# Performance work log

Measured on AMD Instinct MI355X. Metric: run time of the kernel, lower is better.

The kernel has to match this reference:

```python
import jax, jax.numpy as jnp
import numpy as np

B, S, D, H, R = 2, 2048, 1024, 16, 4
HD = D // H  # 64


def _linear_params(key, din, dout):
    k1, k2 = jax.random.split(key)
    bound = 1.0 / np.sqrt(din)
    w = jax.random.uniform(k1, (din, dout), jnp.float32, -bound, bound)
    b = jax.random.uniform(k2, (dout,), jnp.float32, -bound, bound)
    return w, b


def setup_inputs() -> dict:
    key = jax.random.key(0)
    ks = jax.random.split(key, 10)
    x = jax.random.normal(ks[0], (B, S, D), jnp.float32)
    wq_p, bq_p = _linear_params(ks[1], D, D)
    wk_p, bk_p = _linear_params(ks[2], D, D)
    wv_p, bv_p = _linear_params(ks[3], D, D)
    wo_p, bo_p = _linear_params(ks[4], D, D)
    wq_s, bq_s = _linear_params(ks[5], D, H * R)
    wk_s, bk_s = _linear_params(ks[6], D, H * R)
    wv_s, bv_s = _linear_params(ks[7], D, H * R)
    wo_s, bo_s = _linear_params(ks[8], H * R, D)
    w_cross = jnp.float32(-0.1)
    return {"x": x,
            "wq_p": wq_p, "bq_p": bq_p, "wk_p": wk_p, "bk_p": bk_p,
            "wv_p": wv_p, "bv_p": bv_p, "wo_p": wo_p, "bo_p": bo_p,
            "wq_s": wq_s, "bq_s": bq_s, "wk_s": wk_s, "bk_s": bk_s,
            "wv_s": wv_s, "bv_s": bv_s, "wo_s": wo_s, "bo_s": bo_s,
            "w_cross": w_cross}


def _mha(x, wq, bq, wk, bk, wv, bv, dh, scale):
    b, s, _ = x.shape
    q = (x @ wq + bq).reshape(b, s, H, dh)
    k = (x @ wk + bk).reshape(b, s, H, dh)
    v = (x @ wv + bv).reshape(b, s, H, dh)
    scores = jnp.einsum('bqhd,bkhd->bhqk', q, k) / scale
    attn = jax.nn.softmax(scores, axis=-1)
    out = jnp.einsum('bhqk,bkhd->bqhd', attn, v)
    return out.reshape(b, s, H * dh)


def reference(x, wq_p, bq_p, wk_p, bk_p, wv_p, bv_p, wo_p, bo_p,
              wq_s, bq_s, wk_s, bk_s, wv_s, bv_s, wo_s, bo_s, w_cross):
    primary = _mha(x, wq_p, bq_p, wk_p, bk_p, wv_p, bv_p, HD, np.sqrt(HD)) @ wo_p + bo_p
    secondary = _mha(x, wq_s, bq_s, wk_s, bk_s, wv_s, bv_s, R, np.sqrt(R)) @ wo_s + bo_s
    return primary + w_cross * secondary
```

## Files before the change

### kernel.cpp

```cpp
#include <hip/hip_runtime.h>
#include <stdint.h>

typedef unsigned short u16;
typedef __bf16 bf16x8 __attribute__((ext_vector_type(8)));
typedef float f32x4 __attribute__((ext_vector_type(4)));
typedef u16 u16x8 __attribute__((ext_vector_type(8)));
typedef u16 u16x4 __attribute__((ext_vector_type(4)));
typedef unsigned u32x4 __attribute__((ext_vector_type(4)));


__device__ __forceinline__ u16 f2bf(float f) {
  unsigned u = __builtin_bit_cast(unsigned, f);
  u += 0x7FFFu + ((u >> 16) & 1u);
  return (u16)(u >> 16);
}
__device__ __forceinline__ unsigned cvtpk(float lo, float hi) {
  unsigned r;
  asm("v_cvt_pk_bf16_f32 %0, %1, %2" : "=v"(r) : "v"(lo), "v"(hi));
  return r;
}
__device__ __forceinline__ void gld_lds16(const void* g, void* l) {
  __builtin_amdgcn_global_load_lds((__attribute__((address_space(1))) void*)(g),
                                   (__attribute__((address_space(3))) void*)(l),
                                   16, 0, 0);
}

__global__ __launch_bounds__(256)
void k_prep(const float* __restrict__ x,
            const float* __restrict__ wq_p, const float* __restrict__ wk_p,
            const float* __restrict__ wv_p, const float* __restrict__ wo_p,
            const float* __restrict__ wq_s, const float* __restrict__ wk_s,
            const float* __restrict__ wv_s, const float* __restrict__ wo_s,
            const float* __restrict__ bq_p, const float* __restrict__ bk_p,
            const float* __restrict__ bq_s, const float* __restrict__ bk_s,
            const float* __restrict__ bo_p, const float* __restrict__ bo_s,
            const float* __restrict__ wcr,
            u16* __restrict__ xb, u16* __restrict__ Wall, u16* __restrict__ Wvt,
            u16* __restrict__ Wvst, u16* __restrict__ Bto,
            float* __restrict__ ballqk, float* __restrict__ bfin) {
  const int id = blockIdx.x;
  if (id < 2048) {
    const int i = id * 256 + threadIdx.x;
    const float4* p = reinterpret_cast<const float4*>(x) + (size_t)i * 2;
    float4 a = p[0], b = p[1];
    u16x8 o;
    o[0] = f2bf(a.x); o[1] = f2bf(a.y); o[2] = f2bf(a.z); o[3] = f2bf(a.w);
    o[4] = f2bf(b.x); o[5] = f2bf(b.y); o[6] = f2bf(b.z); o[7] = f2bf(b.w);
    *reinterpret_cast<u16x8*>(xb + (size_t)i * 8) = o;
    return;
  }
  if (id < 6400) {
    __shared__ float tile[32][33];
    const int tx = threadIdx.x & 31, ty = threadIdx.x >> 5;
    const float* src; u16* dst; int N, ldd, n0, k0; float sc = 1.f;
    if (id < 6144) {
      const int tid = id - 2048, job = tid >> 10, t10 = tid & 1023;
      switch (job) {
        case 0: src = wq_p; dst = Wall;                       ldd = 1024; break;
        case 1: src = wk_p; dst = Wall + (size_t)1024 * 1024; ldd = 1024; break;
        case 2: src = wv_p; dst = Wvt;                        ldd = 1024; break;
        default: src = wo_p; dst = Bto;                       ldd = 1088; break;
      }
      N = 1024; n0 = (t10 & 31) * 32; k0 = (t10 >> 5) * 32;
    } else {
      const int tid = id - 6144, job = tid >> 6, t6 = tid & 63;
      int ntx;
      switch (job) {
        case 0: src = wq_s; dst = Wall + (size_t)2048 * 1024; N = 64;   ldd = 1024; ntx = 2; break;
        case 1: src = wk_s; dst = Wall + (size_t)2112 * 1024; N = 64;   ldd = 1024; ntx = 2; break;
        case 2: src = wv_s; dst = Wvst;                       N = 64;   ldd = 1024; ntx = 2; break;
        default: src = wo_s; dst = Bto + 1024;                N = 1024; ldd = 1088; ntx = 32; sc = wcr[0]; break;
      }
      n0 = (t6 % ntx) * 32; k0 = (t6 / ntx) * 32;
    }
    #pragma unroll
    for (int i = 0; i < 4; ++i)
      tile[ty + i * 8][tx] = src[(size_t)(k0 + ty + i * 8) * N + n0 + tx];
    __syncthreads();
    #pragma unroll
    for (int i = 0; i < 4; ++i)
      dst[(size_t)(n0 + ty + i * 8) * ldd + k0 + tx] = f2bf(tile[tx][ty + i * 8] * sc);
    return;
  }
  const int i = (id - 6400) * 256 + threadIdx.x;
  if (i < 1024)       ballqk[i] = bq_p[i];
  else if (i < 2048)  ballqk[i] = bk_p[i - 1024];
  else if (i < 2112)  ballqk[i] = bq_s[i - 2048];
  else if (i < 2176)  ballqk[i] = bk_s[i - 2112];
  if (i < 1024) bfin[i] = bo_p[i] + wcr[0] * bo_s[i];
}

template <int BN, int WAVES_M, int OUTMODE, int OHD>
__device__ __forceinline__
void gemm_body(const u16* __restrict__ A, int lda,
               const u16* __restrict__ Bt, int ldb,
               const float* __restrict__ bias,
               void* __restrict__ Cv, int ldc, int K,
               int bx, int by, u16* sm) {
  constexpr int WM = 128 / WAVES_M;
  constexpr int MF = WM / 16;
  u16* Atile = sm;
  u16* Btile = sm + 8192;
  const int t = threadIdx.x, w = t >> 6;
  const int lane = t & 63, l4 = lane & 15, g = lane >> 4;
  const int wr = (WAVES_M == 4) ? w : (w >> 1);
  const int wc = (WAVES_M == 4) ? 0 : (w & 1);
  const int m0 = bx * 128, n0 = by * BN;

  auto stage = [&](int buf, int kt) {
    const int k0 = kt * 32;
    #pragma unroll
    for (int r = 0; r < 2; ++r) {
      const int slot = r * 256 + t;
      const int row = slot >> 2, blk = slot & 3;
      const int srcb = blk ^ ((row >> 1) & 3);
      gld_lds16(A + (size_t)(m0 + row) * lda + k0 + srcb * 8,
                &Atile[buf * 4096 + (r * 256 + w * 64) * 8]);
    }
    #pragma unroll
    for (int r = 0; r < BN / 64; ++r) {
      const int slot = r * 256 + t;
      const int row = slot >> 2, blk = slot & 3;
      const int srcb = blk ^ ((row >> 1) & 3);
      gld_lds16(Bt + (size_t)(n0 + row) * ldb + k0 + srcb * 8,
                &Btile[buf * (BN * 32) + (r * 256 + w * 64) * 8]);
    }
  };

  const f32x4 vz = {0.f, 0.f, 0.f, 0.f};
  f32x4 acc[MF][4];
  #pragma unroll
  for (int mi = 0; mi < MF; ++mi)
    #pragma unroll
    for (int ni = 0; ni < 4; ++ni) acc[mi][ni] = vz;

  const int nkt = K >> 5;
  stage(0, 0);
  __syncthreads();
  for (int kt = 0; kt < nkt; ++kt) {
    const int cur = kt & 1;
    if (kt + 1 < nkt) stage(cur ^ 1, kt + 1);
    bf16x8 af[MF], bfv[4];
    #pragma unroll
    for (int mi = 0; mi < MF; ++mi) {
      const int row = wr * WM + mi * 16 + l4;
      const int blk = g ^ ((row >> 1) & 3);
      af[mi] = *reinterpret_cast<const bf16x8*>(&Atile[cur * 4096 + row * 32 + blk * 8]);
    }
    #pragma unroll
    for (int ni = 0; ni < 4; ++ni) {
      const int row = wc * 64 + ni * 16 + l4;
      const int blk = g ^ ((row >> 1) & 3);
      bfv[ni] = *reinterpret_cast<const bf16x8*>(&Btile[cur * (BN * 32) + row * 32 + blk * 8]);
    }
    #pragma unroll
    for (int mi = 0; mi < MF; ++mi)
      #pragma unroll
      for (int ni = 0; ni < 4; ++ni)
        acc[mi][ni] = __builtin_amdgcn_mfma_f32_16x16x32_bf16(af[mi], bfv[ni],
                                                              acc[mi][ni], 0, 0, 0);
    __syncthreads();
  }
  #pragma unroll
  for (int mi = 0; mi < MF; ++mi) {
    #pragma unroll
    for (int ni = 0; ni < 4; ++ni) {
      const int grow0 = m0 + wr * WM + mi * 16 + g * 4;
      const int gcol = n0 + wc * 64 + ni * 16 + l4;
      const float bb = bias ? bias[gcol] : 0.f;
      if constexpr (OUTMODE == 1) {
        const int bidx = grow0 >> 11, s0 = grow0 & 2047;
        const int hh = gcol / OHD, dd = gcol % OHD;
        u16x4 ov;
        #pragma unroll
        for (int r = 0; r < 4; ++r) ov[r] = f2bf(acc[mi][ni][r] + bb);
        *reinterpret_cast<u16x4*>((u16*)Cv +
            (size_t)((bidx * 16 + hh) * OHD + dd) * 2048 + s0) = ov;
      } else {
        #pragma unroll
        for (int r = 0; r < 4; ++r) {
          const float v = acc[mi][ni][r] + bb;
          if constexpr (OUTMODE == 0)
            ((u16*)Cv)[(size_t)(grow0 + r) * ldc + gcol] = f2bf(v);
          else
            ((float*)Cv)[(size_t)(grow0 + r) * ldc + gcol] = v;
        }
      }
    }
  }
}

__global__ __launch_bounds__(256, 2)
void k_proj3(const u16* __restrict__ xb, const u16* __restrict__ Wall,
             const u16* __restrict__ Wvt, const u16* __restrict__ Wvst,
             const float* __restrict__ ballqk, const float* __restrict__ bv_p,
             const float* __restrict__ bv_s,
             u16* __restrict__ QKs, u16* __restrict__ Vpt, u16* __restrict__ Vst) {
  __shared__ __attribute__((aligned(16))) u16 sm[16384];
  const int id = blockIdx.x;
  if (id < 544) {
    gemm_body<128, 2, 0, 64>(xb, 1024, Wall, 1024, ballqk, QKs, 2176, 1024,
                             id & 31, id >> 5, sm);
  } else if (id < 800) {
    const int lid = id - 544;
    gemm_body<128, 2, 1, 64>(xb, 1024, Wvt, 1024, bv_p, Vpt, 0, 1024,
                             lid & 31, lid >> 5, sm);
  } else {
    const int lid = id - 800;
    gemm_body<64, 4, 1, 4>(xb, 1024, Wvst, 1024, bv_s, Vst, 0, 1024,
                           lid & 31, lid >> 5, sm);
  }
}

__global__ __launch_bounds__(256, 2)
void k_gemm_final(const u16* __restrict__ A, const u16* __restrict__ Bt,
                  const float* __restrict__ bias, float* __restrict__ C) {
  __shared__ __attribute__((aligned(16))) u16 sm[16384];
  gemm_body<128, 2, 2, 64>(A, 1088, Bt, 1088, bias, C, 1024, 1088,
                           blockIdx.x, blockIdx.y, sm);
}

__global__ __launch_bounds__(256, 2)
void k_attn(const u16* __restrict__ QKs, const u16* __restrict__ Vpt,
            const u16* __restrict__ Vst, u16* __restrict__ Ao) {
  __shared__ __attribute__((aligned(16))) u16 sm[26664];
  const int t = threadIdx.x, w = t >> 6;
  const int lane = t & 63, l4 = lane & 15, g = lane >> 4;
  const int grp = blockIdx.x >> 3, sub = blockIdx.x & 7;

  if ((grp & 1) == 0) {
    u16* Klds = sm;
    u16* Vlds = sm + 8192;
    const int id = (grp >> 1) * 8 + sub;
    const int lin = (id & 7) * 64 + (id >> 3);
    const int qt = lin & 15, hb = lin >> 4;
    const int h = hb & 15, b = hb >> 4;
    const int q0 = qt * 128;

    const u16* Qbase = QKs + (size_t)(b * 2048 + q0) * 2176 + h * 64;
    const u16* Kbase = QKs + (size_t)(b * 2048) * 2176 + 1024 + h * 64;
    const u16* Vbase = Vpt + (size_t)((b * 16 + h) * 64) * 2048;

    #pragma unroll
    for (int r = 0; r < 2; ++r) {
      const int sl = r * 256 + t, row = sl >> 3, blk = sl & 7;
      const int srcb = blk ^ (row & 7);
      const int prow = (row & 32) | (((row >> 2) & 3) << 3) | (((row >> 4) & 1) << 2) | (row & 3);
      gld_lds16(Kbase + (size_t)prow * 2176 + srcb * 8, &Klds[(r * 256 + w * 64) * 8]);
      gld_lds16(Vbase + (size_t)row * 2048 + srcb * 8, &Vlds[(r * 256 + w * 64) * 8]);
    }

    bf16x8 aq[2][2];
    #pragma unroll
    for (int mi = 0; mi < 2; ++mi)
      #pragma unroll
      for (int kd = 0; kd < 2; ++kd)
        aq[mi][kd] = *reinterpret_cast<const bf16x8*>(
            Qbase + (size_t)(w * 32 + mi * 16 + l4) * 2176 + kd * 32 + g * 8);

    __syncthreads();

    const f32x4 vz = {0.f, 0.f, 0.f, 0.f};
    float l_r[2] = {0.f, 0.f};
    f32x4 acc_o[2][4];
    #pragma unroll
    for (int mi = 0; mi < 2; ++mi)
      #pragma unroll
      for (int nd = 0; nd < 4; ++nd) acc_o[mi][nd] = vz;

    for (int kt = 0; kt < 32; ++kt) {
      const int cur = kt & 1;
      if (kt < 31) {
        const int kn = kt + 1;
        #pragma unroll
        for (int r = 0; r < 2; ++r) {
          const int sl = r * 256 + t, row = sl >> 3, blk = sl & 7;
          const int srcb = blk ^ (row & 7);
          const int prow = (row & 32) | (((row >> 2) & 3) << 3) | (((row >> 4) & 1) << 2) | (row & 3);
          gld_lds16(Kbase + (size_t)(kn * 64 + prow) * 2176 + srcb * 8,
                    &Klds[(cur ^ 1) * 4096 + (r * 256 + w * 64) * 8]);
          gld_lds16(Vbase + (size_t)row * 2048 + kn * 64 + srcb * 8,
                    &Vlds[(cur ^ 1) * 4096 + (r * 256 + w * 64) * 8]);
        }
      }
      f32x4 sc[2][4];
      #pragma unroll
      for (int mi = 0; mi < 2; ++mi)
        #pragma unroll
        for (int ni = 0; ni < 4; ++ni) sc[mi][ni] = vz;
      #pragma unroll
      for (int kd = 0; kd < 2; ++kd) {
        bf16x8 bk[4];
        #pragma unroll
        for (int ni = 0; ni < 4; ++ni) {
          const int row = ni * 16 + l4;
          const int blk = (kd * 4 + g) ^ (row & 7);
          bk[ni] = *reinterpret_cast<const bf16x8*>(&Klds[cur * 4096 + row * 64 + blk * 8]);
        }
        __builtin_amdgcn_s_setprio(1);
        #pragma unroll
        for (int mi = 0; mi < 2; ++mi)
          #pragma unroll
          for (int ni = 0; ni < 4; ++ni)
            sc[mi][ni] = __builtin_amdgcn_mfma_f32_16x16x32_bf16(bk[ni], aq[mi][kd],
                                                                 sc[mi][ni], 0, 0, 0);
        __builtin_amdgcn_s_setprio(0);
      }
      unsigned pw[2][4][2];
      #pragma unroll
      for (int mi = 0; mi < 2; ++mi) {
        float rs = 0.f;
        #pragma unroll
        for (int ni = 0; ni < 4; ++ni) {
          const float a0 = __expf(sc[mi][ni][0] * 0.125f);
          const float a1 = __expf(sc[mi][ni][1] * 0.125f);
          const float a2 = __expf(sc[mi][ni][2] * 0.125f);
          const float a3 = __expf(sc[mi][ni][3] * 0.125f);
          rs += (a0 + a1) + (a2 + a3);
          pw[mi][ni][0] = cvtpk(a0, a1);
          pw[mi][ni][1] = cvtpk(a2, a3);
        }
        rs += __shfl_xor(rs, 16);
        rs += __shfl_xor(rs, 32);
        l_r[mi] += rs;
      }
      #pragma unroll
      for (int ks = 0; ks < 2; ++ks) {
        bf16x8 bv[4];
        #pragma unroll
        for (int nd = 0; nd < 4; ++nd) {
          const int row = nd * 16 + l4;
          const int blk = (ks * 4 + g) ^ (row & 7);
          bv[nd] = *reinterpret_cast<const bf16x8*>(&Vlds[cur * 4096 + row * 64 + blk * 8]);
        }
        __builtin_amdgcn_s_setprio(1);
        #pragma unroll
        for (int mi = 0; mi < 2; ++mi) {
          const u32x4 aw = {pw[mi][2 * ks][0], pw[mi][2 * ks][1],
                            pw[mi][2 * ks + 1][0], pw[mi][2 * ks + 1][1]};
          const bf16x8 ap = __builtin_bit_cast(bf16x8, aw);
          #pragma unroll
          for (int nd = 0; nd < 4; ++nd)
            acc_o[mi][nd] = __builtin_amdgcn_mfma_f32_16x16x32_bf16(ap, bv[nd],
                                                                    acc_o[mi][nd], 0, 0, 0);
        }
        __builtin_amdgcn_s_setprio(0);
      }
      __syncthreads();
    }
    float linv[2][4];
    #pragma unroll
    for (int mi = 0; mi < 2; ++mi)
      #pragma unroll
      for (int r = 0; r < 4; ++r) {
        const int src = (lane & 48) + ((lane & 48) >> 2) + r;
        linv[mi][r] = 1.0f / __shfl(l_r[mi], src);
      }
    #pragma unroll
    for (int mi = 0; mi < 2; ++mi)
      #pragma unroll
      for (int nd = 0; nd < 4; ++nd)
        #pragma unroll
        for (int r = 0; r < 4; ++r) {
          const int grow = b * 2048 + q0 + w * 32 + mi * 16 + g * 4 + r;
          const int gcol = h * 64 + nd * 16 + l4;
          Ao[(size_t)grow * 1088 + gcol] = f2bf(acc_o[mi][nd][r] * linv[mi][r]);
        }
    return;
  }

  u16* KsL = sm;
  u16* VtL = sm + 8192;
  u16* Plds = sm + 18472;
  const int sid = (grp >> 1) * 8 + sub;
  const int q0 = (sid & 15) * 128, h = (sid >> 4) & 15, b = sid >> 8;

  const u16* Vsrc = Vst + (size_t)((b * 16 + h) * 4) * 2048;
  #pragma unroll
  for (int r = 0; r < 4; ++r)
    gld_lds16(Vsrc + (size_t)r * 2048 + t * 8, &VtL[r * 2056 + w * 512]);
  {
    u16x8 ones;
    #pragma unroll
    for (int j = 0; j < 8; ++j) ones[j] = 0x3F80;
    *reinterpret_cast<u16x8*>(&VtL[4 * 2056 + t * 8]) = ones;
  }
  #pragma unroll
  for (int i = 0; i < 8; ++i) {
    const int s = i * 256 + t;
    const uint2 kk = *reinterpret_cast<const uint2*>(
        QKs + (size_t)(b * 2048 + s) * 2176 + 2112 + h * 4);
    *reinterpret_cast<uint2*>(&KsL[s * 4]) = kk;
  }
  bf16x8 aq[2];
  #pragma unroll
  for (int mi = 0; mi < 2; ++mi) {
    u16x8 qv = {0, 0, 0, 0, 0, 0, 0, 0};
    if (g == 0) {
      const uint2 qq = *reinterpret_cast<const uint2*>(
          QKs + (size_t)(b * 2048 + q0 + w * 32 + mi * 16 + l4) * 2176 + 2048 + h * 4);
      qv[0] = (u16)(qq.x & 0xffff); qv[1] = (u16)(qq.x >> 16);
      qv[2] = (u16)(qq.y & 0xffff); qv[3] = (u16)(qq.y >> 16);
    }
    aq[mi] = __builtin_bit_cast(bf16x8, qv);
  }
  __syncthreads();

  const f32x4 vz = {0.f, 0.f, 0.f, 0.f};
  f32x4 acc[2];
  acc[0] = vz; acc[1] = vz;

  for (int kt = 0; kt < 32; ++kt) {
    f32x4 sc[2][4];
    bf16x8 bk[4];
    #pragma unroll
    for (int ni = 0; ni < 4; ++ni) {
      u16x8 kv = {0, 0, 0, 0, 0, 0, 0, 0};
      if (g == 0) {
        const uint2 kk = *reinterpret_cast<const uint2*>(
            &KsL[(kt * 64 + ni * 16 + l4) * 4]);
        kv[0] = (u16)(kk.x & 0xffff); kv[1] = (u16)(kk.x >> 16);
        kv[2] = (u16)(kk.y & 0xffff); kv[3] = (u16)(kk.y >> 16);
      }
      bk[ni] = __builtin_bit_cast(bf16x8, kv);
    }
    #pragma unroll
    for (int mi = 0; mi < 2; ++mi)
      #pragma unroll
      for (int ni = 0; ni < 4; ++ni)
        sc[mi][ni] = __builtin_amdgcn_mfma_f32_16x16x32_bf16(aq[mi], bk[ni], vz, 0, 0, 0);
    #pragma unroll
    for (int mi = 0; mi < 2; ++mi)
      #pragma unroll
      for (int r = 0; r < 4; ++r) {
        const int prow = mi * 16 + g * 4 + r;
        #pragma unroll
        for (int ni = 0; ni < 4; ++ni) {
          const float p = __expf(sc[mi][ni][r] * 0.5f);
          const int col = ni * 16 + l4;
          Plds[w * 2048 + prow * 64 + ((col >> 3) ^ (prow & 7)) * 8 + (col & 7)] = f2bf(p);
        }
      }
    asm volatile("s_waitcnt lgkmcnt(0)" ::: "memory");
    #pragma unroll
    for (int ks = 0; ks < 2; ++ks) {
      const int blko = kt * 8 + ks * 4 + g;
      const int vrow = (l4 < 4) ? l4 : 4;
      const bf16x8 bv = *reinterpret_cast<const bf16x8*>(&VtL[vrow * 2056 + blko * 8]);
      #pragma unroll
      for (int mi = 0; mi < 2; ++mi) {
        const int row = mi * 16 + l4;
        const int blk = (ks * 4 + g) ^ (row & 7);
        const bf16x8 ap = *reinterpret_cast<const bf16x8*>(&Plds[w * 2048 + row * 64 + blk * 8]);
        acc[mi] = __builtin_amdgcn_mfma_f32_16x16x32_bf16(ap, bv, acc[mi], 0, 0, 0);
      }
    }
  }
  #pragma unroll
  for (int mi = 0; mi < 2; ++mi)
    #pragma unroll
    for (int r = 0; r < 4; ++r) {
      const float lsum = __shfl(acc[mi][r], (lane & 48) + 4);
      if (l4 < 4) {
        const int grow = b * 2048 + q0 + w * 32 + mi * 16 + g * 4 + r;
        Ao[(size_t)grow * 1088 + 1024 + h * 4 + l4] = f2bf(acc[mi][r] / lsum);
      }
    }
}

extern "C" void kernel_launch(void* const* d_in, const int* in_sizes, int n_in,
                              void* d_out, int out_size, void* d_ws, size_t ws_size,
                              hipStream_t stream) {
  (void)in_sizes; (void)n_in; (void)out_size; (void)ws_size;
  const float* x    = (const float*)d_in[0];
  const float* wq_p = (const float*)d_in[1];
  const float* bq_p = (const float*)d_in[2];
  const float* wk_p = (const float*)d_in[3];
  const float* bk_p = (const float*)d_in[4];
  const float* wv_p = (const float*)d_in[5];
  const float* bv_p = (const float*)d_in[6];
  const float* wo_p = (const float*)d_in[7];
  const float* bo_p = (const float*)d_in[8];
  const float* wq_s = (const float*)d_in[9];
  const float* bq_s = (const float*)d_in[10];
  const float* wk_s = (const float*)d_in[11];
  const float* bk_s = (const float*)d_in[12];
  const float* wv_s = (const float*)d_in[13];
  const float* bv_s = (const float*)d_in[14];
  const float* wo_s = (const float*)d_in[15];
  const float* bo_s = (const float*)d_in[16];
  const float* wcr  = (const float*)d_in[17];

  char* p = (char*)d_ws;
  auto take = [&](size_t bytes) { char* r = p; p += (bytes + 255) & ~(size_t)255; return r; };
  u16* xb      = (u16*)take((size_t)4096 * 1024 * 2);
  u16* Wall    = (u16*)take((size_t)2176 * 1024 * 2);
  u16* Wvt     = (u16*)take((size_t)1024 * 1024 * 2);
  u16* Wvst    = (u16*)take((size_t)64 * 1024 * 2);
  u16* Bto     = (u16*)take((size_t)1024 * 1088 * 2);
  float* ballqk= (float*)take(2176 * 4);
  float* bfin  = (float*)take(1024 * 4);
  u16* QKs     = (u16*)take((size_t)4096 * 2176 * 2);
  u16* Vpt     = (u16*)take((size_t)4096 * 1024 * 2);
  u16* Vst     = (u16*)take((size_t)2 * 16 * 4 * 2048 * 2);
  u16* Ao      = (u16*)take((size_t)4096 * 1088 * 2);

  k_prep<<<6409, 256, 0, stream>>>(x, wq_p, wk_p, wv_p, wo_p, wq_s, wk_s, wv_s, wo_s,
                                   bq_p, bk_p, bq_s, bk_s, bo_p, bo_s, wcr,
                                   xb, Wall, Wvt, Wvst, Bto, ballqk, bfin);

  k_proj3<<<832, 256, 0, stream>>>(xb, Wall, Wvt, Wvst, ballqk, bv_p, bv_s,
                                   QKs, Vpt, Vst);

  k_attn<<<1024, 256, 0, stream>>>(QKs, Vpt, Vst, Ao);

  k_gemm_final<<<dim3(32, 8), 256, 0, stream>>>(Ao, Bto, bfin, (float*)d_out);
}
```

Before: 154.8 us.

## Keep secondary-head softmax probabilities in registers instead of LDS round-trip

In the secondary (head dim 4) attention branch, the QK^T MFMA operands are swapped so the score output layout matches the A-operand layout of the PV MFMA. The exp'd probabilities are packed to bf16 in registers and fed directly, with the K rows permuted in LDS to line up. This removes the per-tile P store/load through LDS and the wait on it. The row-sum trick (a ones row in V) is replaced by explicit shuffle-reduced sums. LDS use shrinks, which could raise occupancy, but the block is shared with the primary branch, so its LDS size is set by the larger path.

```diff
diff --git a/kernel.cpp b/kernel.cpp
--- a/kernel.cpp
+++ b/kernel.cpp
@@ -223,7 +223,7 @@
 __global__ __launch_bounds__(256, 2)
 void k_attn(const u16* __restrict__ QKs, const u16* __restrict__ Vpt,
             const u16* __restrict__ Vst, u16* __restrict__ Ao) {
-  __shared__ __attribute__((aligned(16))) u16 sm[26664];
+  __shared__ __attribute__((aligned(16))) u16 sm[16416];
   const int t = threadIdx.x, w = t >> 6;
   const int lane = t & 63, l4 = lane & 15, g = lane >> 4;
   const int grp = blockIdx.x >> 3, sub = blockIdx.x & 7;
@@ -371,7 +371,6 @@
 
   u16* KsL = sm;
   u16* VtL = sm + 8192;
-  u16* Plds = sm + 18472;
   const int sid = (grp >> 1) * 8 + sub;
   const int q0 = (sid & 15) * 128, h = (sid >> 4) & 15, b = sid >> 8;
 
@@ -379,18 +378,13 @@
   #pragma unroll
   for (int r = 0; r < 4; ++r)
     gld_lds16(Vsrc + (size_t)r * 2048 + t * 8, &VtL[r * 2056 + w * 512]);
-  {
-    u16x8 ones;
-    #pragma unroll
-    for (int j = 0; j < 8; ++j) ones[j] = 0x3F80;
-    *reinterpret_cast<u16x8*>(&VtL[4 * 2056 + t * 8]) = ones;
-  }
   #pragma unroll
   for (int i = 0; i < 8; ++i) {
     const int s = i * 256 + t;
     const uint2 kk = *reinterpret_cast<const uint2*>(
         QKs + (size_t)(b * 2048 + s) * 2176 + 2112 + h * 4);
-    *reinterpret_cast<uint2*>(&KsL[s * 4]) = kk;
+    const int slot = (s & ~31) | (((s >> 2) & 1) << 4) | (((s >> 3) & 3) << 2) | (s & 3);
+    *reinterpret_cast<uint2*>(&KsL[slot * 4]) = kk;
   }
   bf16x8 aq[2];
   #pragma unroll
@@ -407,11 +401,11 @@
   __syncthreads();
 
   const f32x4 vz = {0.f, 0.f, 0.f, 0.f};
+  float l_r[2] = {0.f, 0.f};
   f32x4 acc[2];
   acc[0] = vz; acc[1] = vz;
 
   for (int kt = 0; kt < 32; ++kt) {
-    f32x4 sc[2][4];
     bf16x8 bk[4];
     #pragma unroll
     for (int ni = 0; ni < 4; ++ni) {
@@ -424,34 +418,40 @@
       }
       bk[ni] = __builtin_bit_cast(bf16x8, kv);
     }
+    f32x4 sc[2][4];
     #pragma unroll
     for (int mi = 0; mi < 2; ++mi)
       #pragma unroll
       for (int ni = 0; ni < 4; ++ni)
-        sc[mi][ni] = __builtin_amdgcn_mfma_f32_16x16x32_bf16(aq[mi], bk[ni], vz, 0, 0, 0);
-    #pragma unroll
-    for (int mi = 0; mi < 2; ++mi)
-      #pragma unroll
-      for (int r = 0; r < 4; ++r) {
-        const int prow = mi * 16 + g * 4 + r;
-        #pragma unroll
-        for (int ni = 0; ni < 4; ++ni) {
-          const float p = __expf(sc[mi][ni][r] * 0.5f);
-          const int col = ni * 16 + l4;
-          Plds[w * 2048 + prow * 64 + ((col >> 3) ^ (prow & 7)) * 8 + (col & 7)] = f2bf(p);
-        }
-      }
-    asm volatile("s_waitcnt lgkmcnt(0)" ::: "memory");
+        sc[mi][ni] = __builtin_amdgcn_mfma_f32_16x16x32_bf16(bk[ni], aq[mi], vz, 0, 0, 0);
+    unsigned pw[2][4][2];
+    #pragma unroll
+    for (int mi = 0; mi < 2; ++mi) {
+      float rs = 0.f;
+      #pragma unroll
+      for (int ni = 0; ni < 4; ++ni) {
+        const float a0 = __expf(sc[mi][ni][0] * 0.5f);
+        const float a1 = __expf(sc[mi][ni][1] * 0.5f);
+        const float a2 = __expf(sc[mi][ni][2] * 0.5f);
+        const float a3 = __expf(sc[mi][ni][3] * 0.5f);
+        rs += (a0 + a1) + (a2 + a3);
+        pw[mi][ni][0] = cvtpk(a0, a1);
+        pw[mi][ni][1] = cvtpk(a2, a3);
+      }
+      rs += __shfl_xor(rs, 16);
+      rs += __shfl_xor(rs, 32);
+      l_r[mi] += rs;
+    }
     #pragma unroll
     for (int ks = 0; ks < 2; ++ks) {
       const int blko = kt * 8 + ks * 4 + g;
-      const int vrow = (l4 < 4) ? l4 : 4;
+      const int vrow = l4 & 3;
       const bf16x8 bv = *reinterpret_cast<const bf16x8*>(&VtL[vrow * 2056 + blko * 8]);
       #pragma unroll
       for (int mi = 0; mi < 2; ++mi) {
-        const int row = mi * 16 + l4;
-        const int blk = (ks * 4 + g) ^ (row & 7);
-        const bf16x8 ap = *reinterpret_cast<const bf16x8*>(&Plds[w * 2048 + row * 64 + blk * 8]);
+        const u32x4 aw = {pw[mi][2 * ks][0], pw[mi][2 * ks][1],
+                          pw[mi][2 * ks + 1][0], pw[mi][2 * ks + 1][1]};
+        const bf16x8 ap = __builtin_bit_cast(bf16x8, aw);
         acc[mi] = __builtin_amdgcn_mfma_f32_16x16x32_bf16(ap, bv, acc[mi], 0, 0, 0);
       }
     }
@@ -460,10 +460,11 @@
   for (int mi = 0; mi < 2; ++mi)
     #pragma unroll
     for (int r = 0; r < 4; ++r) {
-      const float lsum = __shfl(acc[mi][r], (lane & 48) + 4);
+      const int src = (lane & 48) + ((lane & 48) >> 2) + r;
+      const float linv = 1.0f / __shfl(l_r[mi], src);
       if (l4 < 4) {
         const int grow = b * 2048 + q0 + w * 32 + mi * 16 + g * 4 + r;
-        Ao[(size_t)grow * 1088 + 1024 + h * 4 + l4] = f2bf(acc[mi][r] / lsum);
+        Ao[(size_t)grow * 1088 + 1024 + h * 4 + l4] = f2bf(acc[mi][r] * linv);
       }
     }
 }
```

After: 152.7 us. Within noise of the previous version (-1.3%).
